# Performance work log

Measured on AMD Instinct MI355X. Metric: run time of the kernel, lower is better.

## Reference

```python
import jax, jax.numpy as jnp
import numpy as np

B, D, R = 4096, 1024, 256
DT = 0.01
DT_SCALE = 1.0

# Yoshida 4th-order coefficients
_W1 = 1.0 / (2.0 - 2.0 ** (1.0 / 3.0))
_W0 = -(2.0 ** (1.0 / 3.0)) / (2.0 - 2.0 ** (1.0 / 3.0))
C1 = _W1 / 2.0
C2 = (_W0 + _W1) / 2.0
C3 = C2
C4 = C1
D1 = _W1
D2 = _W0
D3 = _W1


def setup_inputs() -> dict:
    key = jax.random.key(0)
    k1, k2, k3, k4, k5 = jax.random.split(key, 5)
    x = jax.random.normal(k1, (B, D), dtype=jnp.float32)
    v = jax.random.normal(k2, (B, D), dtype=jnp.float32)
    force = jax.random.normal(k3, (B, D), dtype=jnp.float32)
    # low-rank christoffel factors, scaled for numerical stability
    U = jax.random.normal(k4, (R, D), dtype=jnp.float32) * (1.0 / np.sqrt(D))
    W = jax.random.normal(k5, (D, R), dtype=jnp.float32) * (1.0 / np.sqrt(R))
    return {"x": x, "v": v, "force": force, "U": U, "W": W}


def _christoffel(tv, tx, U, W):
    # Gamma(v) = W @ (U v)^2  (low-rank quadratic form; x unused, matching
    # the gfn yoshida_fused(U, W) signature)
    h = jnp.einsum("rd,bd->br", U, tv)  # [B, R]
    return jnp.einsum("dr,br->bd", W, h * h)  # [B, D]


def reference(x, v, force, U, W):
    dt = DT * DT_SCALE

    def acceleration(tx, tv):
        return -_christoffel(tv, tx, U, W) + force

    x1 = x + C1 * dt * v
    v1 = v + D1 * dt * acceleration(x1, v)
    x2 = x1 + C2 * dt * v1
    v2 = v1 + D2 * dt * acceleration(x2, v1)
    x3 = x2 + C3 * dt * v2
    v3 = v2 + D3 * dt * acceleration(x3, v2)
    x_final = x3 + C4 * dt * v3
    return (x_final, v3)
```

## Files before the change

kernel.cpp:

```cpp
#include <hip/hip_runtime.h>


#define BSZ 4096
#define DD 1024
#define RR 256
#define NCOPY 4
#define COPY_BYTES (512u * 1024u)

typedef unsigned char uchar;
typedef long long i64;
typedef __attribute__((ext_vector_type(2))) long i64x2;
typedef __attribute__((ext_vector_type(4))) float f32x4;
typedef __attribute__((ext_vector_type(4))) unsigned int uint4v;
typedef __attribute__((ext_vector_type(4))) _Float16 f16x4;

__device__ inline unsigned int f2q4(float a, float b, float c, float d) {
    int lo = __builtin_amdgcn_cvt_pk_fp8_f32(a, b, 0, false);
    int hi = __builtin_amdgcn_cvt_pk_fp8_f32(c, d, lo, true);
    return (unsigned int)hi;
}
__device__ inline uchar f2q1(float x) {
    return (uchar)(__builtin_amdgcn_cvt_pk_fp8_f32(x, x, 0, false) & 0xff);
}

__global__ __launch_bounds__(256) void pack_uw_kernel(
    const float* __restrict__ U, const float* __restrict__ W,
    uchar* __restrict__ ws)
{
    const int g = blockIdx.x * 256 + threadIdx.x;
    const float* src;
    size_t off;
    float sc;
    if (g < 16384) {
        const int l = g & 63, p = (g >> 6) & 15, nt = g >> 10;
        src = U + (size_t)(nt * 16 + (l & 15)) * DD + p * 64 + (l >> 4) * 8;
        off = ((size_t)nt << 14) + (p << 10) + (l << 4);
        sc = 8.0f;
    } else {
        const int g2 = g - 16384;
        const int l = g2 & 63, p = (g2 >> 6) & 3, dt_ = g2 >> 8;
        src = W + (size_t)(dt_ * 16 + (l & 15)) * RR + p * 64 + (l >> 4) * 8;
        off = (size_t)(256 * 1024) + ((size_t)dt_ << 12) + (p << 10) + (l << 4);
        sc = 16.0f;
    }
    const float4 x0 = *reinterpret_cast<const float4*>(src);
    const float4 x1 = *reinterpret_cast<const float4*>(src + 4);
    const float4 y0 = *reinterpret_cast<const float4*>(src + 32);
    const float4 y1 = *reinterpret_cast<const float4*>(src + 36);
    uint4v o;
    o.x = f2q4(sc * x0.x, sc * x0.y, sc * x0.z, sc * x0.w);
    o.y = f2q4(sc * x1.x, sc * x1.y, sc * x1.z, sc * x1.w);
    o.z = f2q4(sc * y0.x, sc * y0.y, sc * y0.z, sc * y0.w);
    o.w = f2q4(sc * y1.x, sc * y1.y, sc * y1.z, sc * y1.w);
    #pragma unroll
    for (int c = 0; c < NCOPY; ++c)
        *reinterpret_cast<uint4v*>(ws + (size_t)c * COPY_BYTES + off) = o;
}

__global__ __launch_bounds__(1024) void yoshida_fused_kernel(
    const float* __restrict__ x_in,
    const float* __restrict__ v_in,
    const float* __restrict__ force,
    const uchar* __restrict__ ws,
    float* __restrict__ x_out,
    float* __restrict__ v_out)
{
    __shared__ __align__(16) uchar vS[16][1040];
    __shared__ __align__(16) uchar H2S[16][272];
    __shared__ __align__(16) _Float16 fS[16][1032];
    __shared__ __align__(16) float xaS[16][1028];

    const int tid = threadIdx.x;
    const int w = tid >> 6, l = tid & 63;
    const int m = l & 15, q = l >> 4;
    const int b0 = blockIdx.x * 16;
    const int d0 = w * 64;

    const uchar* base = ws + (size_t)((blockIdx.x >> 3) & (NCOPY - 1)) * COPY_BYTES;

    constexpr double CBRT2 = 1.2599210498948731647672106072782;
    constexpr double W1c = 1.0 / (2.0 - CBRT2);
    constexpr double W0c = -CBRT2 * W1c;
    constexpr double DTd = 0.01 * 1.0;
    const float dcoef[3] = {(float)(W1c * DTd), (float)(W0c * DTd), (float)(W1c * DTd)};
    const float xcoef[3] = {(float)((W0c + W1c) * 0.5), (float)((W0c + W1c) * 0.5),
                            (float)(W1c * 0.5)};
    const float c1  = (float)(W1c * 0.5);
    const float dtf = (float)DTd;

    const uchar* up = base + ((size_t)w << 14) + (l << 4);
    const uchar* wp = base + 256 * 1024 + ((size_t)(w * 4) << 12) + (l << 4);

    {
        const int row = tid >> 6;
        const int col = (tid & 63) * 16;
        const float* sp = v_in + (size_t)(b0 + row) * DD + col;
        const float4 f0 = *reinterpret_cast<const float4*>(sp);
        const float4 f1 = *reinterpret_cast<const float4*>(sp + 4);
        const float4 f2 = *reinterpret_cast<const float4*>(sp + 8);
        const float4 f3 = *reinterpret_cast<const float4*>(sp + 12);
        uint4v pk;
        pk.x = f2q4(f0.x, f0.y, f0.z, f0.w);
        pk.y = f2q4(f1.x, f1.y, f1.z, f1.w);
        pk.z = f2q4(f2.x, f2.y, f2.z, f2.w);
        pk.w = f2q4(f3.x, f3.y, f3.z, f3.w);
        *reinterpret_cast<uint4v*>(&vS[row][col]) = pk;
    }

    {
        const float* sp = force + (size_t)(b0 + w) * DD;
        #pragma unroll
        for (int c = 0; c < 4; ++c) {
            const float4 f = *reinterpret_cast<const float4*>(sp + l * 4 + c * 256);
            f16x4 h;
            h.x = (_Float16)f.x; h.y = (_Float16)f.y;
            h.z = (_Float16)f.z; h.w = (_Float16)f.w;
            *reinterpret_cast<f16x4*>(&fS[w][l * 4 + c * 256]) = h;
        }
    }

    float vreg[16];
    #pragma unroll
    for (int t = 0; t < 4; ++t)
        #pragma unroll
        for (int i = 0; i < 4; ++i)
            vreg[t * 4 + i] =
                v_in[(size_t)(b0 + q * 4 + i) * DD + d0 + t * 16 + m];

    i64x2 ub[4];
    #pragma unroll
    for (int p = 0; p < 4; ++p)
        ub[p] = *reinterpret_cast<const i64x2*>(up + (p << 10));

    #pragma unroll
    for (int s = 0; s < 3; ++s) {
        __syncthreads();

        f32x4 a0 = {0.f, 0.f, 0.f, 0.f}, a1 = {0.f, 0.f, 0.f, 0.f};
        #pragma unroll
        for (int p = 0; p < 16; ++p) {
            i64x2 nxt;
            if (p < 12)
                nxt = *reinterpret_cast<const i64x2*>(up + ((p + 4) << 10));
            const i64 af0 = *reinterpret_cast<const i64*>(&vS[m][p * 64 + q * 8]);
            const i64 af1 = *reinterpret_cast<const i64*>(&vS[m][p * 64 + 32 + q * 8]);
            a0 = __builtin_amdgcn_mfma_f32_16x16x32_fp8_fp8(af0, ub[p & 3].x, a0, 0, 0, 0);
            a1 = __builtin_amdgcn_mfma_f32_16x16x32_fp8_fp8(af1, ub[p & 3].y, a1, 0, 0, 0);
            if (p < 12)
                ub[p & 3] = nxt;
        }
        #pragma unroll
        for (int i = 0; i < 4; ++i) {
            const float h8 = a0[i] + a1[i];
            H2S[q * 4 + i][w * 16 + m] = f2q1(h8 * h8 * 0.015625f);
        }

        i64x2 wb[2][4];
        #pragma unroll
        for (int t = 0; t < 4; ++t)
            wb[0][t] = *reinterpret_cast<const i64x2*>(wp + (t << 12));

        __syncthreads();

        f32x4 accB[4];
        #pragma unroll
        for (int t = 0; t < 4; ++t) accB[t] = (f32x4){0.f, 0.f, 0.f, 0.f};
        #pragma unroll
        for (int p = 0; p < 4; ++p) {
            if (p < 3) {
                #pragma unroll
                for (int t = 0; t < 4; ++t)
                    wb[(p + 1) & 1][t] = *reinterpret_cast<const i64x2*>(
                        wp + (t << 12) + ((p + 1) << 10));
            }
            const i64 ha0 = *reinterpret_cast<const i64*>(&H2S[m][p * 64 + q * 8]);
            const i64 ha1 = *reinterpret_cast<const i64*>(&H2S[m][p * 64 + 32 + q * 8]);
            #pragma unroll
            for (int t = 0; t < 4; ++t) {
                accB[t] = __builtin_amdgcn_mfma_f32_16x16x32_fp8_fp8(
                              ha0, wb[p & 1][t].x, accB[t], 0, 0, 0);
                accB[t] = __builtin_amdgcn_mfma_f32_16x16x32_fp8_fp8(
                              ha1, wb[p & 1][t].y, accB[t], 0, 0, 0);
            }
        }

        float xreg[16];
        if (s == 2) {
            #pragma unroll
            for (int t = 0; t < 4; ++t)
                #pragma unroll
                for (int i = 0; i < 4; ++i)
                    xreg[t * 4 + i] =
                        x_in[(size_t)(b0 + q * 4 + i) * DD + d0 + t * 16 + m];
        }

        const float ddt = dcoef[s], cx = xcoef[s], gsc = dcoef[s] * 0.0625f;
        #pragma unroll
        for (int t = 0; t < 4; ++t)
            #pragma unroll
            for (int i = 0; i < 4; ++i) {
                const int r = q * 4 + i, c = d0 + t * 16 + m;
                const float ff = (float)fS[r][c];
                const float vold = vreg[t * 4 + i];
                const float vn = vold + ddt * ff - gsc * accB[t][i];
                vreg[t * 4 + i] = vn;
                if (s == 0) {
                    xaS[r][c] = c1 * vold + cx * vn;
                    vS[r][c] = f2q1(vn);
                } else if (s == 1) {
                    xaS[r][c] += cx * vn;
                    vS[r][c] = f2q1(vn);
                } else {
                    const float xa = xaS[r][c] + cx * vn;
                    const size_t g = (size_t)(b0 + r) * DD + c;
                    x_out[g] = xreg[t * 4 + i] + dtf * xa;
                    v_out[g] = vn;
                }
            }

        if (s < 2) {
            #pragma unroll
            for (int p = 0; p < 4; ++p)
                ub[p] = *reinterpret_cast<const i64x2*>(up + (p << 10));
        }
    }
}

extern "C" void kernel_launch(void* const* d_in, const int* in_sizes, int n_in,
                              void* d_out, int out_size, void* d_ws, size_t ws_size,
                              hipStream_t stream) {
    const float* x     = (const float*)d_in[0];
    const float* v     = (const float*)d_in[1];
    const float* force = (const float*)d_in[2];
    const float* U     = (const float*)d_in[3];
    const float* W     = (const float*)d_in[4];

    float* x_out = (float*)d_out;
    float* v_out = x_out + (size_t)BSZ * DD;

    uchar* ws = (uchar*)d_ws;

    pack_uw_kernel<<<dim3(128), dim3(256), 0, stream>>>(U, W, ws);
    yoshida_fused_kernel<<<dim3(BSZ / 16), dim3(1024), 0, stream>>>(
        x, v, force, ws, x_out, v_out);
}
```

Before: 126.2 us.

## Shrink batch tile to 8 rows with 512-thread blocks, two blocks per CU

After: 150.0 us. +18.8%, slower.

```diff
diff --git a/kernel.cpp b/kernel.cpp
--- a/kernel.cpp
+++ b/kernel.cpp
@@ -57,7 +57,7 @@
         *reinterpret_cast<uint4v*>(ws + (size_t)c * COPY_BYTES + off) = o;
 }
 
-__global__ __launch_bounds__(1024) void yoshida_fused_kernel(
+__global__ __launch_bounds__(512, 2) void yoshida_fused_kernel(
     const float* __restrict__ x_in,
     const float* __restrict__ v_in,
     const float* __restrict__ force,
@@ -67,14 +67,16 @@
 {
     __shared__ __align__(16) uchar vS[16][1040];
     __shared__ __align__(16) uchar H2S[16][272];
-    __shared__ __align__(16) _Float16 fS[16][1032];
-    __shared__ __align__(16) float xaS[16][1028];
+    __shared__ __align__(16) _Float16 fS[8][1032];
+    __shared__ __align__(16) float xaS[8][1028];
 
     const int tid = threadIdx.x;
     const int w = tid >> 6, l = tid & 63;
     const int m = l & 15, q = l >> 4;
-    const int b0 = blockIdx.x * 16;
-    const int d0 = w * 64;
+    const int b0 = blockIdx.x * 8;
+    const int d0 = w * 128;
+    const bool act = (l < 32);
+    const int rbase = (q & 1) * 4;
 
     const uchar* base = ws + (size_t)((blockIdx.x >> 3) & (NCOPY - 1)) * COPY_BYTES;
 
@@ -88,13 +90,11 @@
     const float c1  = (float)(W1c * 0.5);
     const float dtf = (float)DTd;
 
-    const uchar* up = base + ((size_t)w << 14) + (l << 4);
-    const uchar* wp = base + 256 * 1024 + ((size_t)(w * 4) << 12) + (l << 4);
+    const uchar* up = base + ((size_t)(2 * w) << 14) + (l << 4);
+    const uchar* wp = base + 256 * 1024 + ((size_t)(w * 8) << 12) + (l << 4);
 
     {
-        const int row = tid >> 6;
-        const int col = (tid & 63) * 16;
-        const float* sp = v_in + (size_t)(b0 + row) * DD + col;
+        const float* sp = v_in + (size_t)(b0 + w) * DD + l * 16;
         const float4 f0 = *reinterpret_cast<const float4*>(sp);
         const float4 f1 = *reinterpret_cast<const float4*>(sp + 4);
         const float4 f2 = *reinterpret_cast<const float4*>(sp + 8);
@@ -104,9 +104,14 @@
         pk.y = f2q4(f1.x, f1.y, f1.z, f1.w);
         pk.z = f2q4(f2.x, f2.y, f2.z, f2.w);
         pk.w = f2q4(f3.x, f3.y, f3.z, f3.w);
-        *reinterpret_cast<uint4v*>(&vS[row][col]) = pk;
-    }
-
+        *reinterpret_cast<uint4v*>(&vS[w][l * 16]) = pk;
+        const uint4v z = {0u, 0u, 0u, 0u};
+        *reinterpret_cast<uint4v*>(&vS[w + 8][l * 16]) = z;
+    }
+    if (tid < 136) {
+        const uint4v z = {0u, 0u, 0u, 0u};
+        *reinterpret_cast<uint4v*>(&H2S[8 + tid / 17][(tid % 17) * 16]) = z;
+    }
     {
         const float* sp = force + (size_t)(b0 + w) * DD;
         #pragma unroll
@@ -119,40 +124,48 @@
         }
     }
 
-    float vreg[16];
+    float vreg[32];
     #pragma unroll
-    for (int t = 0; t < 4; ++t)
+    for (int t = 0; t < 8; ++t)
         #pragma unroll
         for (int i = 0; i < 4; ++i)
             vreg[t * 4 + i] =
-                v_in[(size_t)(b0 + q * 4 + i) * DD + d0 + t * 16 + m];
-
-    i64x2 ub[4];
-    #pragma unroll
-    for (int p = 0; p < 4; ++p)
-        ub[p] = *reinterpret_cast<const i64x2*>(up + (p << 10));
+                v_in[(size_t)(b0 + rbase + i) * DD + d0 + t * 16 + m];
+
+    i64x2 ub[2][2];
+    ub[0][0] = *reinterpret_cast<const i64x2*>(up);
+    ub[0][1] = *reinterpret_cast<const i64x2*>(up + 16384);
 
     #pragma unroll
     for (int s = 0; s < 3; ++s) {
         __syncthreads();
 
-        f32x4 a0 = {0.f, 0.f, 0.f, 0.f}, a1 = {0.f, 0.f, 0.f, 0.f};
+        f32x4 aA00 = {0.f,0.f,0.f,0.f}, aA01 = {0.f,0.f,0.f,0.f};
+        f32x4 aA10 = {0.f,0.f,0.f,0.f}, aA11 = {0.f,0.f,0.f,0.f};
         #pragma unroll
         for (int p = 0; p < 16; ++p) {
-            i64x2 nxt;
-            if (p < 12)
-                nxt = *reinterpret_cast<const i64x2*>(up + ((p + 4) << 10));
+            if (p < 15) {
+                ub[(p + 1) & 1][0] = *reinterpret_cast<const i64x2*>(up + ((p + 1) << 10));
+                ub[(p + 1) & 1][1] = *reinterpret_cast<const i64x2*>(up + 16384 + ((p + 1) << 10));
+            } else if (s < 2) {
+                ub[0][0] = *reinterpret_cast<const i64x2*>(up);
+                ub[0][1] = *reinterpret_cast<const i64x2*>(up + 16384);
+            }
             const i64 af0 = *reinterpret_cast<const i64*>(&vS[m][p * 64 + q * 8]);
             const i64 af1 = *reinterpret_cast<const i64*>(&vS[m][p * 64 + 32 + q * 8]);
-            a0 = __builtin_amdgcn_mfma_f32_16x16x32_fp8_fp8(af0, ub[p & 3].x, a0, 0, 0, 0);
-            a1 = __builtin_amdgcn_mfma_f32_16x16x32_fp8_fp8(af1, ub[p & 3].y, a1, 0, 0, 0);
-            if (p < 12)
-                ub[p & 3] = nxt;
-        }
-        #pragma unroll
-        for (int i = 0; i < 4; ++i) {
-            const float h8 = a0[i] + a1[i];
-            H2S[q * 4 + i][w * 16 + m] = f2q1(h8 * h8 * 0.015625f);
+            aA00 = __builtin_amdgcn_mfma_f32_16x16x32_fp8_fp8(af0, ub[p & 1][0].x, aA00, 0, 0, 0);
+            aA01 = __builtin_amdgcn_mfma_f32_16x16x32_fp8_fp8(af1, ub[p & 1][0].y, aA01, 0, 0, 0);
+            aA10 = __builtin_amdgcn_mfma_f32_16x16x32_fp8_fp8(af0, ub[p & 1][1].x, aA10, 0, 0, 0);
+            aA11 = __builtin_amdgcn_mfma_f32_16x16x32_fp8_fp8(af1, ub[p & 1][1].y, aA11, 0, 0, 0);
+        }
+        if (act) {
+            #pragma unroll
+            for (int i = 0; i < 4; ++i) {
+                const float h8a = aA00[i] + aA01[i];
+                const float h8b = aA10[i] + aA11[i];
+                H2S[q * 4 + i][(2 * w) * 16 + m]     = f2q1(h8a * h8a * 0.015625f);
+                H2S[q * 4 + i][(2 * w + 1) * 16 + m] = f2q1(h8b * h8b * 0.015625f);
+            }
         }
 
         i64x2 wb[2][4];
@@ -162,67 +175,70 @@
 
         __syncthreads();
 
-        f32x4 accB[4];
-        #pragma unroll
-        for (int t = 0; t < 4; ++t) accB[t] = (f32x4){0.f, 0.f, 0.f, 0.f};
-        #pragma unroll
-        for (int p = 0; p < 4; ++p) {
-            if (p < 3) {
+        f32x4 accB[8];
+        #pragma unroll
+        for (int t = 0; t < 8; ++t) accB[t] = (f32x4){0.f, 0.f, 0.f, 0.f};
+        #pragma unroll
+        for (int h = 0; h < 2; ++h) {
+            #pragma unroll
+            for (int p = 0; p < 4; ++p) {
+                if (p < 3) {
+                    #pragma unroll
+                    for (int t = 0; t < 4; ++t)
+                        wb[(p + 1) & 1][t] = *reinterpret_cast<const i64x2*>(
+                            wp + ((h * 4 + t) << 12) + ((p + 1) << 10));
+                } else if (h == 0) {
+                    #pragma unroll
+                    for (int t = 0; t < 4; ++t)
+                        wb[0][t] = *reinterpret_cast<const i64x2*>(wp + ((4 + t) << 12));
+                }
+                const i64 ha0 = *reinterpret_cast<const i64*>(&H2S[m][p * 64 + q * 8]);
+                const i64 ha1 = *reinterpret_cast<const i64*>(&H2S[m][p * 64 + 32 + q * 8]);
                 #pragma unroll
-                for (int t = 0; t < 4; ++t)
-                    wb[(p + 1) & 1][t] = *reinterpret_cast<const i64x2*>(
-                        wp + (t << 12) + ((p + 1) << 10));
-            }
-            const i64 ha0 = *reinterpret_cast<const i64*>(&H2S[m][p * 64 + q * 8]);
-            const i64 ha1 = *reinterpret_cast<const i64*>(&H2S[m][p * 64 + 32 + q * 8]);
-            #pragma unroll
-            for (int t = 0; t < 4; ++t) {
-                accB[t] = __builtin_amdgcn_mfma_f32_16x16x32_fp8_fp8(
-                              ha0, wb[p & 1][t].x, accB[t], 0, 0, 0);
-                accB[t] = __builtin_amdgcn_mfma_f32_16x16x32_fp8_fp8(
-                              ha1, wb[p & 1][t].y, accB[t], 0, 0, 0);
-            }
-        }
-
-        float xreg[16];
+                for (int t = 0; t < 4; ++t) {
+                    accB[h * 4 + t] = __builtin_amdgcn_mfma_f32_16x16x32_fp8_fp8(
+                                          ha0, wb[p & 1][t].x, accB[h * 4 + t], 0, 0, 0);
+                    accB[h * 4 + t] = __builtin_amdgcn_mfma_f32_16x16x32_fp8_fp8(
+                                          ha1, wb[p & 1][t].y, accB[h * 4 + t], 0, 0, 0);
+                }
+            }
+        }
+
+        float xreg[32];
         if (s == 2) {
             #pragma unroll
-            for (int t = 0; t < 4; ++t)
+            for (int t = 0; t < 8; ++t)
                 #pragma unroll
                 for (int i = 0; i < 4; ++i)
                     xreg[t * 4 + i] =
-                        x_in[(size_t)(b0 + q * 4 + i) * DD + d0 + t * 16 + m];
+                        x_in[(size_t)(b0 + rbase + i) * DD + d0 + t * 16 + m];
         }
 
         const float ddt = dcoef[s], cx = xcoef[s], gsc = dcoef[s] * 0.0625f;
         #pragma unroll
-        for (int t = 0; t < 4; ++t)
+        for (int t = 0; t < 8; ++t)
             #pragma unroll
             for (int i = 0; i < 4; ++i) {
-                const int r = q * 4 + i, c = d0 + t * 16 + m;
+                const int r = rbase + i, c = d0 + t * 16 + m;
                 const float ff = (float)fS[r][c];
                 const float vold = vreg[t * 4 + i];
                 const float vn = vold + ddt * ff - gsc * accB[t][i];
                 vreg[t * 4 + i] = vn;
-                if (s == 0) {
-                    xaS[r][c] = c1 * vold + cx * vn;
-                    vS[r][c] = f2q1(vn);
-                } else if (s == 1) {
-                    xaS[r][c] += cx * vn;
-                    vS[r][c] = f2q1(vn);
-                } else {
-                    const float xa = xaS[r][c] + cx * vn;
-                    const size_t g = (size_t)(b0 + r) * DD + c;
-                    x_out[g] = xreg[t * 4 + i] + dtf * xa;
-                    v_out[g] = vn;
+                if (act) {
+                    if (s == 0) {
+                        xaS[r][c] = c1 * vold + cx * vn;
+                        vS[r][c] = f2q1(vn);
+                    } else if (s == 1) {
+                        xaS[r][c] += cx * vn;
+                        vS[r][c] = f2q1(vn);
+                    } else {
+                        const float xa = xaS[r][c] + cx * vn;
+                        const size_t g = (size_t)(b0 + r) * DD + c;
+                        x_out[g] = xreg[t * 4 + i] + dtf * xa;
+                        v_out[g] = vn;
+                    }
                 }
             }
-
-        if (s < 2) {
-            #pragma unroll
-            for (int p = 0; p < 4; ++p)
-                ub[p] = *reinterpret_cast<const i64x2*>(up + (p << 10));
-        }
     }
 }
 
@@ -241,6 +257,6 @@
     uchar* ws = (uchar*)d_ws;
 
     pack_uw_kernel<<<dim3(128), dim3(256), 0, stream>>>(U, W, ws);
-    yoshida_fused_kernel<<<dim3(BSZ / 16), dim3(1024), 0, stream>>>(
+    yoshida_fused_kernel<<<dim3(BSZ / 8), dim3(512), 0, stream>>>(
         x, v, force, ws, x_out, v_out);
 }
```
